# Kernel optimization log

Measured on AMD Instinct MI355X. Metric: run time of the kernel, lower is better.

Reference implementation:

```python
import jax, jax.numpy as jnp
import numpy as np

SPATIAL = [(80, 80), (40, 40), (20, 20), (10, 10)]  # 640px img, strides 8/16/32/64
BS, LQ, NH, HD, NPTS = 32, 300, 8, 32, 4
EMB = NH * HD
SUMP = NPTS * len(SPATIAL)  # total sampling points per head = 16
OFFSET_SCALE = 0.5


def grid_sample_bilinear(img, grid):
    """torch F.grid_sample(mode='bilinear', padding_mode='zeros', align_corners=False).
    img: [N, C, H, W], grid: [N, Lq, P, 2] (x, y) in [-1, 1] -> [N, C, Lq, P]."""
    N, C, H, W = img.shape
    Lq, P = grid.shape[1], grid.shape[2]
    x = (grid[..., 0] + 1.0) * 0.5 * W - 0.5
    y = (grid[..., 1] + 1.0) * 0.5 * H - 0.5
    x0 = jnp.floor(x).astype(jnp.int32)
    y0 = jnp.floor(y).astype(jnp.int32)
    fx = x - x0
    fy = y - y0
    flat = img.reshape(N, C, H * W)

    def gather(ix, iy):
        valid = (ix >= 0) & (ix < W) & (iy >= 0) & (iy < H)
        idx = jnp.clip(iy, 0, H - 1) * W + jnp.clip(ix, 0, W - 1)
        v = jnp.take_along_axis(flat, idx.reshape(N, 1, Lq * P), axis=2)
        v = v.reshape(N, C, Lq, P)
        return jnp.where(valid[:, None, :, :], v, 0.0)

    w00 = ((1.0 - fx) * (1.0 - fy))[:, None]
    w10 = (fx * (1.0 - fy))[:, None]
    w01 = ((1.0 - fx) * fy)[:, None]
    w11 = (fx * fy)[:, None]
    return (gather(x0, y0) * w00 + gather(x0 + 1, y0) * w10
            + gather(x0, y0 + 1) * w01 + gather(x0 + 1, y0 + 1) * w11)


def setup_inputs() -> dict:
    key = jax.random.key(0)
    ks = jax.random.split(key, 5)
    total = sum(h * w for h, w in SPATIAL)  # 8500
    query = jax.random.normal(ks[0], (BS, LQ, EMB), jnp.float32)
    reference_points = jax.random.uniform(ks[1], (BS, LQ, 1, 4), dtype=jnp.float32)
    value = jax.random.normal(ks[2], (BS, NH, HD, total), jnp.float32)
    W_off = jax.random.normal(ks[3], (EMB, NH * SUMP * 2), jnp.float32) * 0.01
    # _reset_parameters rotated-grid bias
    thetas = np.arange(NH, dtype=np.float32) * (2.0 * np.pi / NH)
    g = np.stack([np.cos(thetas), np.sin(thetas)], -1)
    g = g / np.abs(g).max(-1, keepdims=True)
    g = np.tile(g.reshape(NH, 1, 2), (1, SUMP, 1))
    scal = np.concatenate([np.arange(1, NPTS + 1) for _ in SPATIAL]).reshape(1, -1, 1)
    b_off = jnp.asarray((g * scal).reshape(-1), jnp.float32)
    W_attn = jax.random.normal(ks[4], (EMB, NH * SUMP), jnp.float32) * 0.02
    b_attn = jnp.zeros((NH * SUMP,), jnp.float32)
    vss = np.asarray(SPATIAL, np.int32)
    return dict(query=query, reference_points=reference_points, value=value,
                value_spatial_shapes=vss, W_off=W_off, b_off=b_off,
                W_attn=W_attn, b_attn=b_attn)


def reference(query, reference_points, value, value_spatial_shapes, W_off, b_off, W_attn, b_attn):
    shapes = [(int(h), int(w)) for h, w in np.asarray(value_spatial_shapes)]  # static
    bs, Lq, _ = query.shape
    off = (query @ W_off + b_off).reshape(bs, Lq, NH, SUMP, 2)
    attn = jax.nn.softmax((query @ W_attn + b_attn).reshape(bs, Lq, NH, SUMP), axis=-1)
    nps = jnp.full((SUMP, 1), 1.0 / NPTS, query.dtype)  # num_points_scale
    # 4-dim reference points (cxcywh): loc = cxy + off * scale * wh * offset_scale
    loc = (reference_points[:, :, None, :, :2]
           + off * nps * reference_points[:, :, None, :, 2:] * OFFSET_SCALE)
    grids = (2.0 * loc - 1.0).transpose(0, 2, 1, 3, 4).reshape(bs * NH, Lq, SUMP, 2)
    hd = value.shape[2]
    samples = []
    sp, pt = 0, 0
    for (h, w) in shapes:
        v_l = value[:, :, :, sp:sp + h * w].reshape(bs * NH, hd, h, w)
        g_l = grids[:, :, pt:pt + NPTS]
        samples.append(grid_sample_bilinear(v_l, g_l))
        sp += h * w
        pt += NPTS
    samp = jnp.concatenate(samples, axis=-1)  # [bs*NH, hd, Lq, SUMP]
    aw = attn.transpose(0, 2, 1, 3).reshape(bs * NH, 1, Lq, SUMP)
    out = (samp * aw).sum(-1).reshape(bs, NH * hd, Lq).transpose(0, 2, 1)
    return out  # [bs, Lq, EMB]
```

## Files before the change

### kernel.cpp

```cpp
#include <hip/hip_runtime.h>
#include <hip/hip_bf16.h>

#define BS    32
#define LQ    300
#define NH    8
#define HD    32
#define NPTS  4
#define EMB   256
#define SUMP  16
#define TOTAL 8500
#define NROWS (BS*LQ)

__global__ __launch_bounds__(256) void k_transpose(const float* __restrict__ value,
                                                   __hip_bfloat16* __restrict__ vt) {
    __shared__ float tile[32][33];
    const int bh = blockIdx.y;
    const int s0 = blockIdx.x * 32;
    const int t  = threadIdx.x;
    const int tx = t & 31;
    const int ty = t >> 5;

    const float* src = value + (size_t)bh * HD * TOTAL;
#pragma unroll
    for (int i = 0; i < 4; ++i) {
        int c = ty + 8 * i;
        int s = s0 + tx;
        tile[tx][c] = (s < TOTAL) ? src[(size_t)c * TOTAL + s] : 0.f;
    }
    __syncthreads();

    const int cq = t & 7;
    const int sl = t >> 3;
    const int s  = s0 + sl;
    if (s < TOTAL) {
        ushort4 u;
        __hip_bfloat16 h0 = __float2bfloat16(tile[sl][4 * cq + 0]);
        __hip_bfloat16 h1 = __float2bfloat16(tile[sl][4 * cq + 1]);
        __hip_bfloat16 h2 = __float2bfloat16(tile[sl][4 * cq + 2]);
        __hip_bfloat16 h3 = __float2bfloat16(tile[sl][4 * cq + 3]);
        u.x = *(unsigned short*)&h0;
        u.y = *(unsigned short*)&h1;
        u.z = *(unsigned short*)&h2;
        u.w = *(unsigned short*)&h3;
        *(ushort4*)(vt + (size_t)bh * TOTAL * HD + (size_t)s * HD + 4 * cq) = u;
    }
}

__global__ __launch_bounds__(256) void k_gemm(const float* __restrict__ query,
                                              const float* __restrict__ W_off,
                                              const float* __restrict__ b_off,
                                              const float* __restrict__ W_attn,
                                              const float* __restrict__ b_attn,
                                              float* __restrict__ raw) {
    __shared__ float As[64][68];
    __shared__ float Bs[64][68];

    const int t  = threadIdx.x;
    const int mt = blockIdx.x;
    const int nt = blockIdx.y;

    const float* W;
    const float* bias;
    int ncols, col0;
    if (nt < 4) { W = W_off;  bias = b_off;  ncols = 256; col0 = nt * 64; }
    else        { W = W_attn; bias = b_attn; ncols = 128; col0 = (nt - 4) * 64; }

    const int m0 = mt * 64;
    const int ty = t >> 4;
    const int tx = t & 15;

    float acc[4][4] = {};

    for (int kc = 0; kc < EMB; kc += 64) {
#pragma unroll
        for (int i = 0; i < 16; ++i) {
            int m = (t >> 6) + 4 * i;
            int k = t & 63;
            As[m][k] = query[(size_t)(m0 + m) * EMB + kc + k];
        }
#pragma unroll
        for (int i = 0; i < 16; ++i) {
            int k = (t >> 6) + 4 * i;
            int n = t & 63;
            Bs[k][n] = W[(size_t)(kc + k) * ncols + col0 + n];
        }
        __syncthreads();
#pragma unroll
        for (int k = 0; k < 64; ++k) {
            float4 b4 = *(const float4*)&Bs[k][tx * 4];
            float a;
            a = As[ty * 4 + 0][k];
            acc[0][0] += a * b4.x; acc[0][1] += a * b4.y; acc[0][2] += a * b4.z; acc[0][3] += a * b4.w;
            a = As[ty * 4 + 1][k];
            acc[1][0] += a * b4.x; acc[1][1] += a * b4.y; acc[1][2] += a * b4.z; acc[1][3] += a * b4.w;
            a = As[ty * 4 + 2][k];
            acc[2][0] += a * b4.x; acc[2][1] += a * b4.y; acc[2][2] += a * b4.z; acc[2][3] += a * b4.w;
            a = As[ty * 4 + 3][k];
            acc[3][0] += a * b4.x; acc[3][1] += a * b4.y; acc[3][2] += a * b4.z; acc[3][3] += a * b4.w;
        }
        __syncthreads();
    }

#pragma unroll
    for (int i = 0; i < 4; ++i) {
#pragma unroll
        for (int j = 0; j < 4; ++j) {
            int cl = tx * 4 + j;
            raw[(size_t)(m0 + ty * 4 + i) * 384 + nt * 64 + cl] = acc[i][j] + bias[col0 + cl];
        }
    }
}

__global__ __launch_bounds__(128) void k_post(const float* __restrict__ raw,
                                              const float* __restrict__ refp,
                                              float* __restrict__ locbuf,
                                              float* __restrict__ attnbuf) {
    __shared__ float sm[128];
    const int row = blockIdx.x;
    const int t   = threadIdx.x;
    const int h   = t >> 4;
    const int p   = t & 15;

    float logit = raw[(size_t)row * 384 + 256 + t];
    sm[t] = logit;
    __syncthreads();
    float mx = -3.0e38f;
#pragma unroll
    for (int i = 0; i < 16; ++i) mx = fmaxf(mx, sm[h * 16 + i]);
    float e = __expf(logit - mx);
    __syncthreads();
    sm[t] = e;
    __syncthreads();
    float s = 0.f;
#pragma unroll
    for (int i = 0; i < 16; ++i) s += sm[h * 16 + i];
    attnbuf[(size_t)row * 128 + t] = e / s;

    float ox = raw[(size_t)row * 384 + 2 * t];
    float oy = raw[(size_t)row * 384 + 2 * t + 1];
    float4 rp = *(const float4*)&refp[(size_t)row * 4];
    int lvl = p >> 2;
    float Wl = (float)(80 >> lvl);
    float lx = rp.x + ox * 0.25f * rp.z * 0.5f;
    float ly = rp.y + oy * 0.25f * rp.w * 0.5f;
    locbuf[((size_t)row * 128 + t) * 2 + 0] = lx * Wl - 0.5f;
    locbuf[((size_t)row * 128 + t) * 2 + 1] = ly * Wl - 0.5f;
}

__global__ __launch_bounds__(256) void k_sample(const __hip_bfloat16* __restrict__ vt,
                                                const float* __restrict__ locbuf,
                                                const float* __restrict__ attnbuf,
                                                float* __restrict__ out) {
    const int wid  = (blockIdx.x * 256 + threadIdx.x) >> 6;
    const int lane = threadIdx.x & 63;
    const int ph   = lane >> 5;
    const int cid  = (lane >> 3) & 3;
    const int cg   = lane & 7;
    const int dx   = cid & 1;
    const int dy   = cid >> 1;

    const int q  = wid % LQ;
    const int bh = wid / LQ;
    const int b  = bh >> 3;
    const int h  = bh & 7;
    const int row = b * LQ + q;

    const __hip_bfloat16* slice = vt + (size_t)bh * TOTAL * HD;
    const float* lp = locbuf + ((size_t)row * 128 + h * 16) * 2;
    const float* ap = attnbuf + (size_t)row * 128 + h * 16;

    const int ppre = lane & 15;
    float2 xy = *(const float2*)(lp + 2 * ppre);
    float awl = ap[ppre];

    float4 acc = {0.f, 0.f, 0.f, 0.f};
#pragma unroll
    for (int i = 0; i < 8; ++i) {
        const int lvl = i >> 1;
        const int Wl  = 80 >> lvl;
        const int sp  = (lvl == 0) ? 0 : (lvl == 1) ? 6400 : (lvl == 2) ? 8000 : 8400;

        int p = 2 * i + ph;
        float x = __shfl(xy.x, p, 64);
        float y = __shfl(xy.y, p, 64);
        float aw = __shfl(awl, p, 64);

        x = fminf(fmaxf(x, -1.0e4f), 1.0e4f);
        y = fminf(fmaxf(y, -1.0e4f), 1.0e4f);
        float xf = floorf(x), yf = floorf(y);
        int x0 = (int)xf, y0 = (int)yf;
        float fx = x - xf, fy = y - yf;

        int xi = x0 + dx;
        int yi = y0 + dy;
        bool valid = ((unsigned)xi < (unsigned)Wl) & ((unsigned)yi < (unsigned)Wl);
        float wx = dx ? fx : 1.f - fx;
        float wy = dy ? fy : 1.f - fy;
        float wc = valid ? aw * wx * wy : 0.f;

        int xc = min(max(xi, 0), Wl - 1);
        int yc = min(max(yi, 0), Wl - 1);

        const uint2 v = *(const uint2*)(slice + ((size_t)(sp + yc * Wl + xc) * HD + 4 * cg));
        float f0 = __uint_as_float(v.x << 16);
        float f1 = __uint_as_float(v.x & 0xffff0000u);
        float f2 = __uint_as_float(v.y << 16);
        float f3 = __uint_as_float(v.y & 0xffff0000u);

        acc.x += wc * f0;
        acc.y += wc * f1;
        acc.z += wc * f2;
        acc.w += wc * f3;
    }

#pragma unroll
    for (int m = 8; m <= 32; m <<= 1) {
        acc.x += __shfl_xor(acc.x, m, 64);
        acc.y += __shfl_xor(acc.y, m, 64);
        acc.z += __shfl_xor(acc.z, m, 64);
        acc.w += __shfl_xor(acc.w, m, 64);
    }

    if (lane < 8)
        *(float4*)(out + (size_t)row * EMB + h * HD + 4 * cg) = acc;
}

extern "C" void kernel_launch(void* const* d_in, const int* in_sizes, int n_in,
                              void* d_out, int out_size, void* d_ws, size_t ws_size,
                              hipStream_t stream) {
    const float* query  = (const float*)d_in[0];
    const float* refp   = (const float*)d_in[1];
    const float* value  = (const float*)d_in[2];
    const float* W_off  = (const float*)d_in[4];
    const float* b_off  = (const float*)d_in[5];
    const float* W_attn = (const float*)d_in[6];
    const float* b_attn = (const float*)d_in[7];
    float* out = (float*)d_out;

    char* ws = (char*)d_ws;
    __hip_bfloat16* vt  = (__hip_bfloat16*)ws;
    float* raw     = (float*)(ws + 139264000);
    float* locbuf  = (float*)(ws + 154009600);
    float* attnbuf = (float*)(ws + 163840000);

    k_transpose<<<dim3((TOTAL + 31) / 32, BS * NH), 256, 0, stream>>>(value, vt);
    k_gemm<<<dim3(NROWS / 64, 6), 256, 0, stream>>>(query, W_off, b_off, W_attn, b_attn, raw);
    k_post<<<NROWS, 128, 0, stream>>>(raw, refp, locbuf, attnbuf);
    k_sample<<<(BS * NH * LQ) / 4, 256, 0, stream>>>(vt, locbuf, attnbuf, out);
}
```

Before: 497.9 us.

## Merge transpose and projection GEMM into one launch, fold softmax into sampler

The value transpose-to-bf16 and the query projection GEMM now run as separate block ranges of a single kernel, so they overlap and one launch is saved. The transpose drops its shared-memory tile in favour of direct float4 loads, with each thread writing four rows. The GEMM tile loads are vectorised to float4. The post kernel is removed: softmax and location computation move into the sampling kernel using wave shuffles, which drops the loc/attn intermediate buffers and one launch. The trade-off is that each head's softmax is recomputed per wave and the transpose's memory accesses are less coalesced.

After: 453.4 us. -8.9%, faster.

```diff
diff --git a/kernel.cpp b/kernel.cpp
--- a/kernel.cpp
+++ b/kernel.cpp
@@ -5,48 +5,22 @@
 #define LQ    300
 #define NH    8
 #define HD    32
-#define NPTS  4
 #define EMB   256
-#define SUMP  16
 #define TOTAL 8500
 #define NROWS (BS*LQ)
 
-__global__ __launch_bounds__(256) void k_transpose(const float* __restrict__ value,
-                                                   __hip_bfloat16* __restrict__ vt) {
-    __shared__ float tile[32][33];
-    const int bh = blockIdx.y;
-    const int s0 = blockIdx.x * 32;
-    const int t  = threadIdx.x;
-    const int tx = t & 31;
-    const int ty = t >> 5;
-
-    const float* src = value + (size_t)bh * HD * TOTAL;
-#pragma unroll
-    for (int i = 0; i < 4; ++i) {
-        int c = ty + 8 * i;
-        int s = s0 + tx;
-        tile[tx][c] = (s < TOTAL) ? src[(size_t)c * TOTAL + s] : 0.f;
-    }
-    __syncthreads();
-
-    const int cq = t & 7;
-    const int sl = t >> 3;
-    const int s  = s0 + sl;
-    if (s < TOTAL) {
-        ushort4 u;
-        __hip_bfloat16 h0 = __float2bfloat16(tile[sl][4 * cq + 0]);
-        __hip_bfloat16 h1 = __float2bfloat16(tile[sl][4 * cq + 1]);
-        __hip_bfloat16 h2 = __float2bfloat16(tile[sl][4 * cq + 2]);
-        __hip_bfloat16 h3 = __float2bfloat16(tile[sl][4 * cq + 3]);
-        u.x = *(unsigned short*)&h0;
-        u.y = *(unsigned short*)&h1;
-        u.z = *(unsigned short*)&h2;
-        u.w = *(unsigned short*)&h3;
-        *(ushort4*)(vt + (size_t)bh * TOTAL * HD + (size_t)s * HD + 4 * cq) = u;
-    }
-}
-
-__global__ __launch_bounds__(256) void k_gemm(const float* __restrict__ query,
+#define GEMM_BLOCKS   900
+#define TP_BLK_PER_BH 67
+#define TP_BLOCKS     (BS*NH*TP_BLK_PER_BH)
+
+static __device__ __forceinline__ unsigned short to_bf16(float x) {
+    __hip_bfloat16 h = __float2bfloat16(x);
+    return *(unsigned short*)&h;
+}
+
+__global__ __launch_bounds__(256) void k_prep(const float* __restrict__ value,
+                                              __hip_bfloat16* __restrict__ vt,
+                                              const float* __restrict__ query,
                                               const float* __restrict__ W_off,
                                               const float* __restrict__ b_off,
                                               const float* __restrict__ W_attn,
@@ -54,10 +28,37 @@
                                               float* __restrict__ raw) {
     __shared__ float As[64][68];
     __shared__ float Bs[64][68];
-
-    const int t  = threadIdx.x;
-    const int mt = blockIdx.x;
-    const int nt = blockIdx.y;
+    const int t = threadIdx.x;
+
+    if (blockIdx.x >= GEMM_BLOCKS) {
+        const int bx2 = blockIdx.x - GEMM_BLOCKS;
+        const int bh  = bx2 / TP_BLK_PER_BH;
+        const int blk = bx2 % TP_BLK_PER_BH;
+        const int cq  = t & 7;
+        const int sq  = t >> 3;
+        const int s   = blk * 128 + 4 * sq;
+        if (s < TOTAL) {
+            const float* src = value + (size_t)bh * HD * TOTAL;
+            float4 f[4];
+#pragma unroll
+            for (int j = 0; j < 4; ++j)
+                f[j] = *(const float4*)(src + (size_t)(4 * cq + j) * TOTAL + s);
+            __hip_bfloat16* dst = vt + (size_t)bh * TOTAL * HD + (size_t)s * HD + 4 * cq;
+#pragma unroll
+            for (int j2 = 0; j2 < 4; ++j2) {
+                ushort4 u;
+                u.x = to_bf16(((const float*)&f[0])[j2]);
+                u.y = to_bf16(((const float*)&f[1])[j2]);
+                u.z = to_bf16(((const float*)&f[2])[j2]);
+                u.w = to_bf16(((const float*)&f[3])[j2]);
+                *(ushort4*)(dst + (size_t)j2 * HD) = u;
+            }
+        }
+        return;
+    }
+
+    const int mt = blockIdx.x % 150;
+    const int nt = blockIdx.x / 150;
 
     const float* W;
     const float* bias;
@@ -72,17 +73,23 @@
     float acc[4][4] = {};
 
     for (int kc = 0; kc < EMB; kc += 64) {
-#pragma unroll
-        for (int i = 0; i < 16; ++i) {
-            int m = (t >> 6) + 4 * i;
-            int k = t & 63;
-            As[m][k] = query[(size_t)(m0 + m) * EMB + kc + k];
-        }
-#pragma unroll
-        for (int i = 0; i < 16; ++i) {
-            int k = (t >> 6) + 4 * i;
-            int n = t & 63;
-            Bs[k][n] = W[(size_t)(kc + k) * ncols + col0 + n];
+        {
+            const int k4 = t & 15;
+            const int mb = t >> 4;
+#pragma unroll
+            for (int i = 0; i < 4; ++i) {
+                int m = mb + 16 * i;
+                *(float4*)&As[m][4 * k4] =
+                    *(const float4*)&query[(size_t)(m0 + m) * EMB + kc + 4 * k4];
+            }
+            const int n4 = t & 15;
+            const int kb = t >> 4;
+#pragma unroll
+            for (int i = 0; i < 4; ++i) {
+                int k = kb + 16 * i;
+                *(float4*)&Bs[k][4 * n4] =
+                    *(const float4*)&W[(size_t)(kc + k) * ncols + col0 + 4 * n4];
+            }
         }
         __syncthreads();
 #pragma unroll
@@ -111,45 +118,9 @@
     }
 }
 
-__global__ __launch_bounds__(128) void k_post(const float* __restrict__ raw,
-                                              const float* __restrict__ refp,
-                                              float* __restrict__ locbuf,
-                                              float* __restrict__ attnbuf) {
-    __shared__ float sm[128];
-    const int row = blockIdx.x;
-    const int t   = threadIdx.x;
-    const int h   = t >> 4;
-    const int p   = t & 15;
-
-    float logit = raw[(size_t)row * 384 + 256 + t];
-    sm[t] = logit;
-    __syncthreads();
-    float mx = -3.0e38f;
-#pragma unroll
-    for (int i = 0; i < 16; ++i) mx = fmaxf(mx, sm[h * 16 + i]);
-    float e = __expf(logit - mx);
-    __syncthreads();
-    sm[t] = e;
-    __syncthreads();
-    float s = 0.f;
-#pragma unroll
-    for (int i = 0; i < 16; ++i) s += sm[h * 16 + i];
-    attnbuf[(size_t)row * 128 + t] = e / s;
-
-    float ox = raw[(size_t)row * 384 + 2 * t];
-    float oy = raw[(size_t)row * 384 + 2 * t + 1];
-    float4 rp = *(const float4*)&refp[(size_t)row * 4];
-    int lvl = p >> 2;
-    float Wl = (float)(80 >> lvl);
-    float lx = rp.x + ox * 0.25f * rp.z * 0.5f;
-    float ly = rp.y + oy * 0.25f * rp.w * 0.5f;
-    locbuf[((size_t)row * 128 + t) * 2 + 0] = lx * Wl - 0.5f;
-    locbuf[((size_t)row * 128 + t) * 2 + 1] = ly * Wl - 0.5f;
-}
-
 __global__ __launch_bounds__(256) void k_sample(const __hip_bfloat16* __restrict__ vt,
-                                                const float* __restrict__ locbuf,
-                                                const float* __restrict__ attnbuf,
+                                                const float* __restrict__ raw,
+                                                const float* __restrict__ refp,
                                                 float* __restrict__ out) {
     const int wid  = (blockIdx.x * 256 + threadIdx.x) >> 6;
     const int lane = threadIdx.x & 63;
@@ -158,21 +129,34 @@
     const int cg   = lane & 7;
     const int dx   = cid & 1;
     const int dy   = cid >> 1;
-
-    const int q  = wid % LQ;
-    const int bh = wid / LQ;
-    const int b  = bh >> 3;
-    const int h  = bh & 7;
+    const int p16  = lane & 15;
+
+    const int q   = wid % LQ;
+    const int bh  = wid / LQ;
+    const int b   = bh >> 3;
+    const int h   = bh & 7;
     const int row = b * LQ + q;
 
+    const float* rrow = raw + (size_t)row * 384;
+    float  logit = rrow[256 + h * 16 + p16];
+    float2 off   = *(const float2*)(rrow + 2 * (h * 16 + p16));
+    float4 rp    = *(const float4*)(refp + (size_t)row * 4);
+
+    float mx = logit;
+#pragma unroll
+    for (int m = 1; m < 16; m <<= 1) mx = fmaxf(mx, __shfl_xor(mx, m, 64));
+    float e = __expf(logit - mx);
+    float sum = e;
+#pragma unroll
+    for (int m = 1; m < 16; m <<= 1) sum += __shfl_xor(sum, m, 64);
+    float awl = e / sum;
+
+    const int lvlp = p16 >> 2;
+    const float Wlp = (float)(80 >> lvlp);
+    float lx = (rp.x + off.x * 0.125f * rp.z) * Wlp - 0.5f;
+    float ly = (rp.y + off.y * 0.125f * rp.w) * Wlp - 0.5f;
+
     const __hip_bfloat16* slice = vt + (size_t)bh * TOTAL * HD;
-    const float* lp = locbuf + ((size_t)row * 128 + h * 16) * 2;
-    const float* ap = attnbuf + (size_t)row * 128 + h * 16;
-
-    const int ppre = lane & 15;
-    float2 xy = *(const float2*)(lp + 2 * ppre);
-    float awl = ap[ppre];
-
     float4 acc = {0.f, 0.f, 0.f, 0.f};
 #pragma unroll
     for (int i = 0; i < 8; ++i) {
@@ -181,8 +165,8 @@
         const int sp  = (lvl == 0) ? 0 : (lvl == 1) ? 6400 : (lvl == 2) ? 8000 : 8400;
 
         int p = 2 * i + ph;
-        float x = __shfl(xy.x, p, 64);
-        float y = __shfl(xy.y, p, 64);
+        float x  = __shfl(lx,  p, 64);
+        float y  = __shfl(ly,  p, 64);
         float aw = __shfl(awl, p, 64);
 
         x = fminf(fmaxf(x, -1.0e4f), 1.0e4f);
@@ -202,15 +186,10 @@
         int yc = min(max(yi, 0), Wl - 1);
 
         const uint2 v = *(const uint2*)(slice + ((size_t)(sp + yc * Wl + xc) * HD + 4 * cg));
-        float f0 = __uint_as_float(v.x << 16);
-        float f1 = __uint_as_float(v.x & 0xffff0000u);
-        float f2 = __uint_as_float(v.y << 16);
-        float f3 = __uint_as_float(v.y & 0xffff0000u);
-
-        acc.x += wc * f0;
-        acc.y += wc * f1;
-        acc.z += wc * f2;
-        acc.w += wc * f3;
+        acc.x += wc * __uint_as_float(v.x << 16);
+        acc.y += wc * __uint_as_float(v.x & 0xffff0000u);
+        acc.z += wc * __uint_as_float(v.y << 16);
+        acc.w += wc * __uint_as_float(v.y & 0xffff0000u);
     }
 
 #pragma unroll
@@ -238,13 +217,10 @@
     float* out = (float*)d_out;
 
     char* ws = (char*)d_ws;
-    __hip_bfloat16* vt  = (__hip_bfloat16*)ws;
-    float* raw     = (float*)(ws + 139264000);
-    float* locbuf  = (float*)(ws + 154009600);
-    float* attnbuf = (float*)(ws + 163840000);
-
-    k_transpose<<<dim3((TOTAL + 31) / 32, BS * NH), 256, 0, stream>>>(value, vt);
-    k_gemm<<<dim3(NROWS / 64, 6), 256, 0, stream>>>(query, W_off, b_off, W_attn, b_attn, raw);
-    k_post<<<NROWS, 128, 0, stream>>>(raw, refp, locbuf, attnbuf);
-    k_sample<<<(BS * NH * LQ) / 4, 256, 0, stream>>>(vt, locbuf, attnbuf, out);
-}
+    __hip_bfloat16* vt = (__hip_bfloat16*)ws;
+    float* raw = (float*)(ws + 139264000);
+
+    k_prep<<<GEMM_BLOCKS + TP_BLOCKS, 256, 0, stream>>>(value, vt, query,
+                                                        W_off, b_off, W_attn, b_attn, raw);
+    k_sample<<<(BS * NH * LQ) / 4, 256, 0, stream>>>(vt, raw, refp, out);
+}
```
